# Optimization experiments

Measured on AMD Instinct MI355X. Metric: run time of the kernel, lower is better.

Reference implementation:

```python
import jax, jax.numpy as jnp
import numpy as np

H = 128          # num_hidden
NUM_IN = 256     # 2*H: h_E (H) + gathered neighbor h_V (H)
SCALE = 30.0
LN_EPS = 1e-5


def _ln(x, g, b):
    mu = jnp.mean(x, axis=-1, keepdims=True)
    var = jnp.mean((x - mu) ** 2, axis=-1, keepdims=True)
    return (x - mu) * jax.lax.rsqrt(var + LN_EPS) * g + b


def _gather_nodes(nodes, idx):
    # nodes: [B,L,C], idx: [B,L,K] -> [B,L,K,C]
    B = nodes.shape[0]
    return nodes[jnp.arange(B)[:, None, None], idx]


def _mlp3(x, W1, b1, W2, b2, W3, b3):
    h = jax.nn.gelu(x @ W1 + b1, approximate=False)
    h = jax.nn.gelu(h @ W2 + b2, approximate=False)
    return h @ W3 + b3


def setup_inputs() -> dict:
    key = jax.random.key(0)
    ks = jax.random.split(key, 16)
    B, L, K = 2, 2048, 48
    s = 0.02
    inp = {
        "h_V": jax.random.normal(ks[0], (B, L, H), jnp.float32),
        "h_E": jax.random.normal(ks[1], (B, L, K, H), jnp.float32),
        "E_idx": jax.random.randint(ks[2], (B, L, K), 0, L, jnp.int32),
        "mask_V": jnp.ones((B, L), jnp.float32),
        "mask_attend": jnp.ones((B, L, K), jnp.float32),
        # node-update MLP
        "W1": jax.random.normal(ks[3], (H + NUM_IN, H), jnp.float32) * s,
        "b1": jnp.zeros((H,), jnp.float32),
        "W2": jax.random.normal(ks[4], (H, H), jnp.float32) * s,
        "b2": jnp.zeros((H,), jnp.float32),
        "W3": jax.random.normal(ks[5], (H, H), jnp.float32) * s,
        "b3": jnp.zeros((H,), jnp.float32),
        # edge-update MLP
        "W11": jax.random.normal(ks[6], (H + NUM_IN, H), jnp.float32) * s,
        "b11": jnp.zeros((H,), jnp.float32),
        "W12": jax.random.normal(ks[7], (H, H), jnp.float32) * s,
        "b12": jnp.zeros((H,), jnp.float32),
        "W13": jax.random.normal(ks[8], (H, H), jnp.float32) * s,
        "b13": jnp.zeros((H,), jnp.float32),
        # position-wise FFN (H -> 4H -> H)
        "Win": jax.random.normal(ks[9], (H, 4 * H), jnp.float32) * s,
        "bin": jnp.zeros((4 * H,), jnp.float32),
        "Wout": jax.random.normal(ks[10], (4 * H, H), jnp.float32) * s,
        "bout": jnp.zeros((H,), jnp.float32),
        # LayerNorms
        "g1": jnp.ones((H,), jnp.float32), "be1": jnp.zeros((H,), jnp.float32),
        "g2": jnp.ones((H,), jnp.float32), "be2": jnp.zeros((H,), jnp.float32),
        "g3": jnp.ones((H,), jnp.float32), "be3": jnp.zeros((H,), jnp.float32),
    }
    return inp


def reference(h_V, h_E, E_idx, mask_V, mask_attend,
              W1, b1, W2, b2, W3, b3,
              W11, b11, W12, b12, W13, b13,
              Win, bin, Wout, bout,
              g1, be1, g2, be2, g3, be3):
    K = h_E.shape[-2]
    # --- node update: gather, concat, 3-layer MLP, masked mean-sum, LN residual ---
    h_nbr = _gather_nodes(h_V, E_idx)                               # [B,L,K,H]
    h_V_exp = jnp.broadcast_to(h_V[:, :, None, :], h_nbr.shape)     # [B,L,K,H]
    h_EV = jnp.concatenate([h_V_exp, h_E, h_nbr], axis=-1)          # [B,L,K,3H]
    h_msg = _mlp3(h_EV, W1, b1, W2, b2, W3, b3)                     # [B,L,K,H]
    h_msg = mask_attend[..., None] * h_msg
    dh = jnp.sum(h_msg, axis=-2) / SCALE                            # [B,L,H]
    h_V = _ln(h_V + dh, g1, be1)
    # position-wise FFN + LN residual
    dh = jax.nn.gelu(h_V @ Win + bin, approximate=False) @ Wout + bout
    h_V = _ln(h_V + dh, g2, be2)
    h_V = mask_V[..., None] * h_V
    # --- edge update ---
    h_nbr = _gather_nodes(h_V, E_idx)
    h_V_exp = jnp.broadcast_to(h_V[:, :, None, :], h_nbr.shape)
    h_EV = jnp.concatenate([h_V_exp, h_E, h_nbr], axis=-1)
    h_msg = _mlp3(h_EV, W11, b11, W12, b12, W13, b13)
    h_E = _ln(h_E + h_msg, g3, be3)
    return (h_V, h_E)
```

## Files before the change

### kernel.cpp

```cpp
#include <hip/hip_runtime.h>
#include <hip/hip_bf16.h>

typedef __attribute__((ext_vector_type(8))) short short8;
typedef __attribute__((ext_vector_type(4))) float f32x4;

__device__ inline short f2bf(float f) {
    unsigned u = __builtin_bit_cast(unsigned, f);
    u += 0x7fffu + ((u >> 16) & 1u);
    return (short)(u >> 16);
}
__device__ inline float bf2f(short s) {
    return __builtin_bit_cast(float, ((unsigned)(unsigned short)s) << 16);
}
__device__ inline float bflo(unsigned u) { return __builtin_bit_cast(float, u << 16); }
__device__ inline float bfhi(unsigned u) { return __builtin_bit_cast(float, u & 0xffff0000u); }
__device__ inline unsigned cvt_pk_bf16(float a, float b) {
    unsigned r;
    asm("v_cvt_pk_bf16_f32 %0, %1, %2" : "=v"(r) : "v"(a), "v"(b));
    return r;
}
__device__ inline float gelu_fast(float x) {
    float z = x * (1.0f + 0.044715f * x * x);
    float e = __expf(1.5957691216f * z);
    return x - x * __builtin_amdgcn_rcpf(e + 1.0f);
}
__device__ inline float wred(float s) {
#pragma unroll
    for (int o = 32; o; o >>= 1) s += __shfl_xor(s, o, 64);
    return s;
}

__global__ void pack_all_kernel(const float* __restrict__ W1, const float* __restrict__ W2,
                                const float* __restrict__ W3, const float* __restrict__ W11,
                                const float* __restrict__ W12, const float* __restrict__ W13,
                                const float* __restrict__ Win, const float* __restrict__ Wout,
                                short* __restrict__ out) {
    int b = blockIdx.x;
    if (b < 80) {
        int which = b >> 3;
        const float* Ws[10] = {W1 + 128 * 128, W2, W3, W11 + 128 * 128, W12, W13,
                               W1, W1 + 256 * 128, W11, W11 + 256 * 128};
        const float* W = Ws[which];
        int i = (b & 7) * 256 + threadIdx.x;
        int lane = i & 63, tile = i >> 6;
        int kt = tile & 3, nt = tile >> 2;
        int n = nt * 16 + (lane & 15);
        int k0 = kt * 32 + (lane >> 4) * 8;
        short8 v;
#pragma unroll
        for (int j = 0; j < 8; ++j) v[j] = f2bf(W[(size_t)(k0 + j) * 128 + n]);
        *(short8*)(out + (size_t)which * 16384 + (size_t)i * 8) = v;
    } else if (b < 112) {
        int i = (b - 80) * 256 + threadIdx.x;
        int lane = i & 63, tile = i >> 6;
        int kt = tile & 3, nt = tile >> 2;
        int n = nt * 16 + (lane & 15);
        int k0 = kt * 32 + (lane >> 4) * 8;
        short8 v;
#pragma unroll
        for (int j = 0; j < 8; ++j) v[j] = f2bf(Win[(size_t)(k0 + j) * 512 + n]);
        *(short8*)(out + 163840 + (size_t)i * 8) = v;
    } else {
        int i = (b - 112) * 256 + threadIdx.x;
        int lane = i & 63, tile = i >> 6;
        int kt = tile & 15, nt = tile >> 4;
        int n = nt * 16 + (lane & 15);
        int k0 = kt * 32 + (lane >> 4) * 8;
        short8 v;
#pragma unroll
        for (int j = 0; j < 8; ++j) v[j] = f2bf(Wout[(size_t)(k0 + j) * 128 + n]);
        *(short8*)(out + 229376 + (size_t)i * 8) = v;
    }
}

__global__ __launch_bounds__(256) void node_pre_kernel(
    const float* __restrict__ hV, const short8* __restrict__ Bs,
    const short8* __restrict__ Bn, const float* __restrict__ bias,
    float* __restrict__ Ys, short* __restrict__ Yn) {
    int n0 = blockIdx.x * 16;
    int tid = threadIdx.x, lane = tid & 63, w = tid >> 6;
    __shared__ __align__(16) short A_sw[16 * 128];
    {
        int off = tid * 8;
        int r = off >> 7, c0 = off & 127;
        const float* src = hV + (size_t)n0 * 128 + off;
        float4 f0 = *(const float4*)(src);
        float4 f1 = *(const float4*)(src + 4);
        uint4 u;
        u.x = cvt_pk_bf16(f0.x, f0.y); u.y = cvt_pk_bf16(f0.z, f0.w);
        u.z = cvt_pk_bf16(f1.x, f1.y); u.w = cvt_pk_bf16(f1.z, f1.w);
        *(uint4*)((char*)A_sw + r * 256 + ((c0 * 2) ^ ((r & 7) << 4))) = u;
    }
    __syncthreads();
    const short8* Bp = (w < 2) ? Bs : Bn;
    f32x4 acc[4];
#pragma unroll
    for (int n2 = 0; n2 < 4; ++n2) acc[n2] = (f32x4){0.f, 0.f, 0.f, 0.f};
#pragma unroll
    for (int kt = 0; kt < 4; ++kt) {
        int row = lane & 15;
        int kb = (kt * 32 + (lane >> 4) * 8) * 2;
        short8 a = *(const short8*)((const char*)A_sw + row * 256 + (kb ^ ((row & 7) << 4)));
#pragma unroll
        for (int n2 = 0; n2 < 4; ++n2) {
            int ntl = (w & 1) * 4 + n2;
            short8 bf = Bp[(ntl * 4 + kt) * 64 + lane];
            acc[n2] = __builtin_amdgcn_mfma_f32_16x16x32_bf16(a, bf, acc[n2], 0, 0, 0);
        }
    }
    if (w < 2) {
#pragma unroll
        for (int n2 = 0; n2 < 4; ++n2) {
            int col = ((w & 1) * 4 + n2) * 16 + (lane & 15);
            float bv = bias[col];
#pragma unroll
            for (int i = 0; i < 4; ++i) {
                int row = (lane >> 4) * 4 + i;
                Ys[(size_t)(n0 + row) * 128 + col] = acc[n2][i] + bv;
            }
        }
    } else {
#pragma unroll
        for (int n2 = 0; n2 < 4; ++n2) {
            int col = ((w & 1) * 4 + n2) * 16 + (lane & 15);
#pragma unroll
            for (int i = 0; i < 4; ++i) {
                int row = (lane >> 4) * 4 + i;
                Yn[(size_t)(n0 + row) * 128 + col] = f2bf(acc[n2][i]);
            }
        }
    }
}


__device__ inline void gemm48_a(const short* A_sw, const short8* __restrict__ Wp,
                                int w, int lane, f32x4 acc[3][2]) {
#pragma unroll
    for (int mt = 0; mt < 3; ++mt)
#pragma unroll
        for (int n2 = 0; n2 < 2; ++n2) acc[mt][n2] = (f32x4){0.f, 0.f, 0.f, 0.f};
#pragma unroll
    for (int kt = 0; kt < 4; ++kt) {
        short8 a[3];
        int kb = (kt * 32 + (lane >> 4) * 8) * 2;
#pragma unroll
        for (int mt = 0; mt < 3; ++mt) {
            int row = mt * 16 + (lane & 15);
            a[mt] = *(const short8*)((const char*)A_sw + row * 256 + (kb ^ ((row & 7) << 4)));
        }
#pragma unroll
        for (int n2 = 0; n2 < 2; ++n2) {
            short8 bf = Wp[((w * 2 + n2) * 4 + kt) * 64 + lane];
#pragma unroll
            for (int mt = 0; mt < 3; ++mt)
                acc[mt][n2] = __builtin_amdgcn_mfma_f32_16x16x32_bf16(a[mt], bf, acc[mt][n2], 0, 0, 0);
        }
    }
}

__device__ inline void gemm48_swz(const short* A_sw, const short8* __restrict__ Wp,
                                  int w, int lane, f32x4 acc[2][3]) {
#pragma unroll
    for (int m2 = 0; m2 < 2; ++m2)
#pragma unroll
        for (int nt = 0; nt < 3; ++nt) acc[m2][nt] = (f32x4){0.f, 0.f, 0.f, 0.f};
#pragma unroll
    for (int kt = 0; kt < 4; ++kt) {
        int kb = (kt * 32 + (lane >> 4) * 8) * 2;
        short8 e[3];
#pragma unroll
        for (int nt = 0; nt < 3; ++nt) {
            int row = nt * 16 + (lane & 15);
            e[nt] = *(const short8*)((const char*)A_sw + row * 256 + (kb ^ ((row & 7) << 4)));
        }
#pragma unroll
        for (int m2 = 0; m2 < 2; ++m2) {
            short8 wf = Wp[((w * 2 + m2) * 4 + kt) * 64 + lane];
#pragma unroll
            for (int nt = 0; nt < 3; ++nt)
                acc[m2][nt] = __builtin_amdgcn_mfma_f32_16x16x32_bf16(wf, e[nt], acc[m2][nt], 0, 0, 0);
        }
    }
}

__device__ inline void gemm48_swz1(const short* A_sw, const short8* __restrict__ Wp,
                                   int ft, int lane, f32x4 acc[3]) {
#pragma unroll
    for (int nt = 0; nt < 3; ++nt) acc[nt] = (f32x4){0.f, 0.f, 0.f, 0.f};
#pragma unroll
    for (int kt = 0; kt < 4; ++kt) {
        int kb = (kt * 32 + (lane >> 4) * 8) * 2;
        short8 e[3];
#pragma unroll
        for (int nt = 0; nt < 3; ++nt) {
            int row = nt * 16 + (lane & 15);
            e[nt] = *(const short8*)((const char*)A_sw + row * 256 + (kb ^ ((row & 7) << 4)));
        }
        short8 wf = Wp[(ft * 4 + kt) * 64 + lane];
#pragma unroll
        for (int nt = 0; nt < 3; ++nt)
            acc[nt] = __builtin_amdgcn_mfma_f32_16x16x32_bf16(wf, e[nt], acc[nt], 0, 0, 0);
    }
}

__device__ inline void gemm48_a1(const short* A_sw, const short8* __restrict__ Wp,
                                 int ft, int lane, f32x4 acc[3]) {
#pragma unroll
    for (int mt = 0; mt < 3; ++mt) acc[mt] = (f32x4){0.f, 0.f, 0.f, 0.f};
#pragma unroll
    for (int kt = 0; kt < 4; ++kt) {
        short8 a[3];
        int kb = (kt * 32 + (lane >> 4) * 8) * 2;
#pragma unroll
        for (int mt = 0; mt < 3; ++mt) {
            int row = mt * 16 + (lane & 15);
            a[mt] = *(const short8*)((const char*)A_sw + row * 256 + (kb ^ ((row & 7) << 4)));
        }
        short8 bf = Wp[(ft * 4 + kt) * 64 + lane];
#pragma unroll
        for (int mt = 0; mt < 3; ++mt)
            acc[mt] = __builtin_amdgcn_mfma_f32_16x16x32_bf16(a[mt], bf, acc[mt], 0, 0, 0);
    }
}

__device__ inline void stage_hE(const float* __restrict__ Eb, short* A_sw, int tid) {
#pragma unroll
    for (int i = 0; i < 3; ++i) {
        int e = tid + i * 256;
        int r = e >> 4, c0 = (e & 15) * 8;
        float4 f0 = *(const float4*)(Eb + r * 128 + c0);
        float4 f1 = *(const float4*)(Eb + r * 128 + c0 + 4);
        uint4 u;
        u.x = cvt_pk_bf16(f0.x, f0.y); u.y = cvt_pk_bf16(f0.z, f0.w);
        u.z = cvt_pk_bf16(f1.x, f1.y); u.w = cvt_pk_bf16(f1.z, f1.w);
        *(uint4*)((char*)A_sw + r * 256 + ((c0 * 2) ^ ((r & 7) << 4))) = u;
    }
}

__device__ inline void stage_hE512(const float* __restrict__ Eb, short* A_sw, int tid) {
#pragma unroll
    for (int i = 0; i < 2; ++i) {
        int e = tid + i * 512;
        if (i == 1 && e >= 768) break;
        int r = e >> 4, c0 = (e & 15) * 8;
        float4 f0 = *(const float4*)(Eb + r * 128 + c0);
        float4 f1 = *(const float4*)(Eb + r * 128 + c0 + 4);
        uint4 u;
        u.x = cvt_pk_bf16(f0.x, f0.y); u.y = cvt_pk_bf16(f0.z, f0.w);
        u.z = cvt_pk_bf16(f1.x, f1.y); u.w = cvt_pk_bf16(f1.z, f1.w);
        *(uint4*)((char*)A_sw + r * 256 + ((c0 * 2) ^ ((r & 7) << 4))) = u;
    }
}

__device__ inline void gather_Yn(const short* __restrict__ Yng, const int* __restrict__ Eidx,
                                 int node, int bb, int tid, short* Ygb) {
    if (tid < 192) {
        int r = tid >> 2, q = tid & 3;
        int idx = Eidx[node * 48 + r];
        const short8* src = (const short8*)(Yng + ((size_t)bb * 2048 + idx) * 128 + q * 32);
        short8* dst = (short8*)(Ygb + r * 136 + q * 32);
        dst[0] = src[0];
        dst[1] = src[1];
        dst[2] = src[2];
        dst[3] = src[3];
    }
}

__device__ inline void epi_l1(f32x4 acc[2][3], const float* Ysh, const short* Ygb,
                              short* A_sw, int w, int lane) {
#pragma unroll
    for (int m2 = 0; m2 < 2; ++m2) {
        int featb = (w * 2 + m2) * 16 + ((lane >> 4) << 2);
        float ys0 = Ysh[featb], ys1 = Ysh[featb + 1];
        float ys2 = Ysh[featb + 2], ys3 = Ysh[featb + 3];
#pragma unroll
        for (int nt = 0; nt < 3; ++nt) {
            int edge = nt * 16 + (lane & 15);
            uint2 yv = *(const uint2*)(Ygb + edge * 136 + featb);
            float v0 = gelu_fast(acc[m2][nt][0] + ys0 + bflo(yv.x));
            float v1 = gelu_fast(acc[m2][nt][1] + ys1 + bfhi(yv.x));
            float v2 = gelu_fast(acc[m2][nt][2] + ys2 + bflo(yv.y));
            float v3 = gelu_fast(acc[m2][nt][3] + ys3 + bfhi(yv.y));
            uint2 pk = {cvt_pk_bf16(v0, v1), cvt_pk_bf16(v2, v3)};
            *(uint2*)((char*)A_sw + edge * 256 + ((featb * 2) ^ ((edge & 7) << 4))) = pk;
        }
    }
}

__device__ inline void epi_l2(f32x4 acc[2][3], const float* __restrict__ b,
                              short* A_sw, int w, int lane) {
#pragma unroll
    for (int m2 = 0; m2 < 2; ++m2) {
        int featb = (w * 2 + m2) * 16 + ((lane >> 4) << 2);
        float b0 = b[featb], b1 = b[featb + 1], b2v = b[featb + 2], b3v = b[featb + 3];
#pragma unroll
        for (int nt = 0; nt < 3; ++nt) {
            int edge = nt * 16 + (lane & 15);
            float v0 = gelu_fast(acc[m2][nt][0] + b0);
            float v1 = gelu_fast(acc[m2][nt][1] + b1);
            float v2 = gelu_fast(acc[m2][nt][2] + b2v);
            float v3 = gelu_fast(acc[m2][nt][3] + b3v);
            uint2 pk = {cvt_pk_bf16(v0, v1), cvt_pk_bf16(v2, v3)};
            *(uint2*)((char*)A_sw + edge * 256 + ((featb * 2) ^ ((edge & 7) << 4))) = pk;
        }
    }
}

__global__ __launch_bounds__(256) void node_msg_kernel(
    const float* __restrict__ hV, const float* __restrict__ hE,
    const int* __restrict__ Eidx, const float* __restrict__ maskAtt,
    const short8* __restrict__ W1bp, const short8* __restrict__ W2p,
    const short8* __restrict__ W3p, const float* __restrict__ b2,
    const float* __restrict__ b3, const float* __restrict__ Ysg,
    const short* __restrict__ Yng, const float* __restrict__ g1,
    const float* __restrict__ be1, float* __restrict__ hv1out) {
    const int node = blockIdx.x;
    const int bb = node >> 11;
    const int tid = threadIdx.x;
    const int lane = tid & 63, w = tid >> 6;

    __shared__ __align__(16) short A_sw[48 * 128];
    __shared__ __align__(16) short Ygb[48 * 136];
    __shared__ float Ysh[128];
    __shared__ float mask_s[48];
    __shared__ float red[8];

    stage_hE(hE + (size_t)node * 6144, A_sw, tid);
    if (tid < 128) Ysh[tid] = Ysg[(size_t)node * 128 + tid];
    if (tid >= 192 && tid < 240) mask_s[tid - 192] = maskAtt[node * 48 + tid - 192];
    gather_Yn(Yng, Eidx, node, bb, tid, Ygb);
    __syncthreads();

    f32x4 acc[2][3];
    gemm48_swz(A_sw, W1bp, w, lane, acc);
    __syncthreads();
    epi_l1(acc, Ysh, Ygb, A_sw, w, lane);
    __syncthreads();
    gemm48_swz(A_sw, W2p, w, lane, acc);
    __syncthreads();
    epi_l2(acc, b2, A_sw, w, lane);
    __syncthreads();

    f32x4 acc3[3][2];
    gemm48_a(A_sw, W3p, w, lane, acc3);
    float u[2];
#pragma unroll
    for (int n2 = 0; n2 < 2; ++n2) {
        int col = (w * 2 + n2) * 16 + (lane & 15);
        float b3c = b3[col];
        float s = 0.f;
#pragma unroll
        for (int mt = 0; mt < 3; ++mt)
#pragma unroll
            for (int i = 0; i < 4; ++i) {
                int row = mt * 16 + (lane >> 4) * 4 + i;
                s += (acc3[mt][n2][i] + b3c) * mask_s[row];
            }
        s += __shfl_xor(s, 16, 64);
        s += __shfl_xor(s, 32, 64);
        u[n2] = hV[(size_t)node * 128 + col] + s * (1.0f / 30.0f);
    }
    float ps = wred(u[0] + u[1]) * 0.25f;
    float pq = wred(u[0] * u[0] + u[1] * u[1]) * 0.25f;
    if (lane == 0) { red[w] = ps; red[4 + w] = pq; }
    __syncthreads();
    float S = red[0] + red[1] + red[2] + red[3];
    float Q = red[4] + red[5] + red[6] + red[7];
    float mu = S * (1.0f / 128.0f);
    float var = Q * (1.0f / 128.0f) - mu * mu;
    float rs = rsqrtf(var + 1e-5f);
    if ((lane >> 4) == 0) {
#pragma unroll
        for (int n2 = 0; n2 < 2; ++n2) {
            int col = (w * 2 + n2) * 16 + (lane & 15);
            hv1out[(size_t)node * 128 + col] = (u[n2] - mu) * rs * g1[col] + be1[col];
        }
    }
}

__global__ __launch_bounds__(256) void ffn_kernel(
    const float* __restrict__ hv1, const short8* __restrict__ Winp,
    const float* __restrict__ binp, const short8* __restrict__ Woutp,
    const float* __restrict__ bout, const float* __restrict__ g2,
    const float* __restrict__ be2, const float* __restrict__ maskV,
    float* __restrict__ hVout) {
    int n0 = blockIdx.x * 16;
    int tid = threadIdx.x, lane = tid & 63, w = tid >> 6;
    __shared__ float X[16 * 128];
    __shared__ __align__(16) short A_sw[16 * 128];
    __shared__ __align__(16) short H_sw[16 * 512];

    {
        int off = tid * 8;
        int r = off >> 7, c0 = off & 127;
        const float* src = hv1 + (size_t)n0 * 128 + off;
        float4 f0 = *(const float4*)(src);
        float4 f1 = *(const float4*)(src + 4);
        *(float4*)(&X[off]) = f0;
        *(float4*)(&X[off + 4]) = f1;
        uint4 u;
        u.x = cvt_pk_bf16(f0.x, f0.y); u.y = cvt_pk_bf16(f0.z, f0.w);
        u.z = cvt_pk_bf16(f1.x, f1.y); u.w = cvt_pk_bf16(f1.z, f1.w);
        *(uint4*)((char*)A_sw + r * 256 + ((c0 * 2) ^ ((r & 7) << 4))) = u;
    }
    __syncthreads();

    f32x4 acc1[8];
#pragma unroll
    for (int n2 = 0; n2 < 8; ++n2) acc1[n2] = (f32x4){0.f, 0.f, 0.f, 0.f};
#pragma unroll
    for (int kt = 0; kt < 4; ++kt) {
        int row = lane & 15;
        int kb = (kt * 32 + (lane >> 4) * 8) * 2;
        short8 a = *(const short8*)((const char*)A_sw + row * 256 + (kb ^ ((row & 7) << 4)));
#pragma unroll
        for (int n2 = 0; n2 < 8; ++n2) {
            short8 bf = Winp[((w * 8 + n2) * 4 + kt) * 64 + lane];
            acc1[n2] = __builtin_amdgcn_mfma_f32_16x16x32_bf16(a, bf, acc1[n2], 0, 0, 0);
        }
    }
#pragma unroll
    for (int n2 = 0; n2 < 8; ++n2) {
        int col = (w * 8 + n2) * 16 + (lane & 15);
        float bv = binp[col];
#pragma unroll
        for (int i = 0; i < 4; ++i) {
            int row = (lane >> 4) * 4 + i;
            float v = gelu_fast(acc1[n2][i] + bv);
            *(short*)((char*)H_sw + row * 1024 + ((col * 2) ^ ((row & 7) << 4))) = f2bf(v);
        }
    }
    __syncthreads();

    f32x4 acc2[2];
    acc2[0] = (f32x4){0.f, 0.f, 0.f, 0.f};
    acc2[1] = (f32x4){0.f, 0.f, 0.f, 0.f};
#pragma unroll
    for (int kt = 0; kt < 16; ++kt) {
        int row = lane & 15;
        int kb = (kt * 32 + (lane >> 4) * 8) * 2;
        short8 a = *(const short8*)((const char*)H_sw + row * 1024 + (kb ^ ((row & 7) << 4)));
#pragma unroll
        for (int n2 = 0; n2 < 2; ++n2) {
            short8 bf = Woutp[((w * 2 + n2) * 16 + kt) * 64 + lane];
            acc2[n2] = __builtin_amdgcn_mfma_f32_16x16x32_bf16(a, bf, acc2[n2], 0, 0, 0);
        }
    }
#pragma unroll
    for (int n2 = 0; n2 < 2; ++n2) {
        int col = (w * 2 + n2) * 16 + (lane & 15);
        float bo = bout[col];
#pragma unroll
        for (int i = 0; i < 4; ++i) {
            int row = (lane >> 4) * 4 + i;
            X[row * 128 + col] += acc2[n2][i] + bo;
        }
    }
    __syncthreads();

#pragma unroll
    for (int p = 0; p < 4; ++p) {
        int r = p * 4 + w;
        float u0 = X[r * 128 + lane], u1 = X[r * 128 + lane + 64];
        float s = wred(u0 + u1);
        float q = wred(u0 * u0 + u1 * u1);
        float mu = s * (1.0f / 128.0f);
        float var = q * (1.0f / 128.0f) - mu * mu;
        float rs = rsqrtf(var + 1e-5f);
        float mv = maskV[n0 + r];
        hVout[(size_t)(n0 + r) * 128 + lane] = mv * ((u0 - mu) * rs * g2[lane] + be2[lane]);
        hVout[(size_t)(n0 + r) * 128 + lane + 64] = mv * ((u1 - mu) * rs * g2[lane + 64] + be2[lane + 64]);
    }
}

__global__ __launch_bounds__(512) void edge_upd_kernel(
    const float* __restrict__ hE, const int* __restrict__ Eidx,
    const short8* __restrict__ W11bp, const short8* __restrict__ W12p,
    const short8* __restrict__ W13p, const float* __restrict__ b12,
    const float* __restrict__ b13, const float* __restrict__ Ysg,
    const short* __restrict__ Yng, const float* __restrict__ g3,
    const float* __restrict__ be3, float* __restrict__ hEout) {
    const int node = blockIdx.x;
    const int bb = node >> 11;
    const int tid = threadIdx.x;
    const int lane = tid & 63, w = tid >> 6;

    __shared__ __align__(16) short A_sw[48 * 128];
    __shared__ __align__(16) short Ygb[48 * 136];
    __shared__ float Ysh[128];

    const float* Eb = hE + (size_t)node * 6144;
    stage_hE512(Eb, A_sw, tid);
    if (tid < 128) Ysh[tid] = Ysg[(size_t)node * 128 + tid];
    gather_Yn(Yng, Eidx, node, bb, tid, Ygb);
    __syncthreads();

    f32x4 acc[3];
    gemm48_swz1(A_sw, W11bp, w, lane, acc);
    __syncthreads();
    {
        int featb = w * 16 + ((lane >> 4) << 2);
        float ys0 = Ysh[featb], ys1 = Ysh[featb + 1];
        float ys2 = Ysh[featb + 2], ys3 = Ysh[featb + 3];
#pragma unroll
        for (int nt = 0; nt < 3; ++nt) {
            int edge = nt * 16 + (lane & 15);
            uint2 yv = *(const uint2*)(Ygb + edge * 136 + featb);
            float v0 = gelu_fast(acc[nt][0] + ys0 + bflo(yv.x));
            float v1 = gelu_fast(acc[nt][1] + ys1 + bfhi(yv.x));
            float v2 = gelu_fast(acc[nt][2] + ys2 + bflo(yv.y));
            float v3 = gelu_fast(acc[nt][3] + ys3 + bfhi(yv.y));
            uint2 pk = {cvt_pk_bf16(v0, v1), cvt_pk_bf16(v2, v3)};
            *(uint2*)((char*)A_sw + edge * 256 + ((featb * 2) ^ ((edge & 7) << 4))) = pk;
        }
    }
    __syncthreads();
    gemm48_swz1(A_sw, W12p, w, lane, acc);
    __syncthreads();
    {
        int featb = w * 16 + ((lane >> 4) << 2);
        float b0 = b12[featb], b1 = b12[featb + 1];
        float b2v = b12[featb + 2], b3v = b12[featb + 3];
#pragma unroll
        for (int nt = 0; nt < 3; ++nt) {
            int edge = nt * 16 + (lane & 15);
            float v0 = gelu_fast(acc[nt][0] + b0);
            float v1 = gelu_fast(acc[nt][1] + b1);
            float v2 = gelu_fast(acc[nt][2] + b2v);
            float v3 = gelu_fast(acc[nt][3] + b3v);
            uint2 pk = {cvt_pk_bf16(v0, v1), cvt_pk_bf16(v2, v3)};
            *(uint2*)((char*)A_sw + edge * 256 + ((featb * 2) ^ ((edge & 7) << 4))) = pk;
        }
    }
    __syncthreads();

    f32x4 acc3[3];
    gemm48_a1(A_sw, W13p, w, lane, acc3);
    {
        int col = w * 16 + (lane & 15);
        float bv = b13[col];
#pragma unroll
        for (int mt = 0; mt < 3; ++mt)
#pragma unroll
            for (int i = 0; i < 4; ++i) {
                int row = mt * 16 + (lane >> 4) * 4 + i;
                float v = acc3[mt][i] + bv + Eb[row * 128 + col];
                Ygb[row * 136 + col] = f2bf(v);
            }
    }
    __syncthreads();

    float* outb = hEout + (size_t)node * 6144;
    float gl0 = g3[lane], gl1 = g3[lane + 64];
    float bl0 = be3[lane], bl1 = be3[lane + 64];
#pragma unroll
    for (int p = 0; p < 6; ++p) {
        int r = p * 8 + w;
        float u0 = bf2f(Ygb[r * 136 + lane]);
        float u1 = bf2f(Ygb[r * 136 + lane + 64]);
        float s = wred(u0 + u1);
        float q = wred(u0 * u0 + u1 * u1);
        float mu = s * (1.0f / 128.0f);
        float var = q * (1.0f / 128.0f) - mu * mu;
        float rs = rsqrtf(var + 1e-5f);
        outb[r * 128 + lane] = (u0 - mu) * rs * gl0 + bl0;
        outb[r * 128 + lane + 64] = (u1 - mu) * rs * gl1 + bl1;
    }
}

extern "C" void kernel_launch(void* const* d_in, const int* in_sizes, int n_in,
                              void* d_out, int out_size, void* d_ws, size_t ws_size,
                              hipStream_t stream) {
    const float* hV      = (const float*)d_in[0];
    const float* hE      = (const float*)d_in[1];
    const int*   Eidx    = (const int*)d_in[2];
    const float* maskV   = (const float*)d_in[3];
    const float* maskAtt = (const float*)d_in[4];
    const float* W1  = (const float*)d_in[5];
    const float* b1  = (const float*)d_in[6];
    const float* W2  = (const float*)d_in[7];
    const float* b2  = (const float*)d_in[8];
    const float* W3  = (const float*)d_in[9];
    const float* b3  = (const float*)d_in[10];
    const float* W11 = (const float*)d_in[11];
    const float* b11 = (const float*)d_in[12];
    const float* W12 = (const float*)d_in[13];
    const float* b12 = (const float*)d_in[14];
    const float* W13 = (const float*)d_in[15];
    const float* b13 = (const float*)d_in[16];
    const float* Win = (const float*)d_in[17];
    const float* binp= (const float*)d_in[18];
    const float* Wout= (const float*)d_in[19];
    const float* bout= (const float*)d_in[20];
    const float* g1  = (const float*)d_in[21];
    const float* be1 = (const float*)d_in[22];
    const float* g2  = (const float*)d_in[23];
    const float* be2 = (const float*)d_in[24];
    const float* g3  = (const float*)d_in[25];
    const float* be3 = (const float*)d_in[26];

    char* ws = (char*)d_ws;
    short* Wpk  = (short*)ws;
    float* Ys   = (float*)(ws + 1048576);
    short* Yn   = (short*)(ws + 1048576 + 2097152);
    float* hv1  = (float*)(ws + 1048576 + 2097152 + 1048576);

    float* hVout = (float*)d_out;
    float* hEout = hVout + 2 * 2048 * 128;

    const int NNODE = 2 * 2048;

    pack_all_kernel<<<144, 256, 0, stream>>>(W1, W2, W3, W11, W12, W13, Win, Wout, Wpk);

    node_pre_kernel<<<NNODE / 16, 256, 0, stream>>>(hV,
        (const short8*)(Wpk + 98304), (const short8*)(Wpk + 114688), b1, Ys, Yn);

    node_msg_kernel<<<NNODE, 256, 0, stream>>>(hV, hE, Eidx, maskAtt,
        (const short8*)(Wpk), (const short8*)(Wpk + 16384), (const short8*)(Wpk + 32768),
        b2, b3, Ys, Yn, g1, be1, hv1);

    ffn_kernel<<<NNODE / 16, 256, 0, stream>>>(hv1,
        (const short8*)(Wpk + 163840), binp, (const short8*)(Wpk + 229376), bout,
        g2, be2, maskV, hVout);

    node_pre_kernel<<<NNODE / 16, 256, 0, stream>>>(hVout,
        (const short8*)(Wpk + 131072), (const short8*)(Wpk + 147456), b11, Ys, Yn);

    edge_upd_kernel<<<NNODE, 512, 0, stream>>>(hE, Eidx,
        (const short8*)(Wpk + 49152), (const short8*)(Wpk + 65536), (const short8*)(Wpk + 81920),
        b12, b13, Ys, Yn, g3, be3, hEout);
}
```

Before: 137.7 us.

## Process two nodes per block in edge update kernel with 96-row GEMM tiles

The edge-update kernel now handles two nodes (96 edges) per 256-thread block instead of one node per 512-thread block. Each wave computes 32 output features across all 96 rows, so every weight fragment loaded is reused across twice as many MFMAs. This also halves the block count. The cost is more shared memory and more accumulator registers per thread, which may reduce occupancy. Node-message helpers are inlined and stage and gather functions are templated, with no change in behaviour.

```diff
diff --git a/kernel.cpp b/kernel.cpp
--- a/kernel.cpp
+++ b/kernel.cpp
@@ -183,49 +183,60 @@
     }
 }
 
-__device__ inline void gemm48_swz1(const short* A_sw, const short8* __restrict__ Wp,
-                                   int ft, int lane, f32x4 acc[3]) {
-#pragma unroll
-    for (int nt = 0; nt < 3; ++nt) acc[nt] = (f32x4){0.f, 0.f, 0.f, 0.f};
+__device__ inline void gemm96_swz(const short* A_sw, const short8* __restrict__ Wp,
+                                  int w, int lane, f32x4 acc[2][6]) {
+#pragma unroll
+    for (int m2 = 0; m2 < 2; ++m2)
+#pragma unroll
+        for (int nt = 0; nt < 6; ++nt) acc[m2][nt] = (f32x4){0.f, 0.f, 0.f, 0.f};
 #pragma unroll
     for (int kt = 0; kt < 4; ++kt) {
         int kb = (kt * 32 + (lane >> 4) * 8) * 2;
-        short8 e[3];
-#pragma unroll
-        for (int nt = 0; nt < 3; ++nt) {
+        short8 e[6];
+#pragma unroll
+        for (int nt = 0; nt < 6; ++nt) {
             int row = nt * 16 + (lane & 15);
             e[nt] = *(const short8*)((const char*)A_sw + row * 256 + (kb ^ ((row & 7) << 4)));
         }
-        short8 wf = Wp[(ft * 4 + kt) * 64 + lane];
-#pragma unroll
-        for (int nt = 0; nt < 3; ++nt)
-            acc[nt] = __builtin_amdgcn_mfma_f32_16x16x32_bf16(wf, e[nt], acc[nt], 0, 0, 0);
-    }
-}
-
-__device__ inline void gemm48_a1(const short* A_sw, const short8* __restrict__ Wp,
-                                 int ft, int lane, f32x4 acc[3]) {
-#pragma unroll
-    for (int mt = 0; mt < 3; ++mt) acc[mt] = (f32x4){0.f, 0.f, 0.f, 0.f};
+#pragma unroll
+        for (int m2 = 0; m2 < 2; ++m2) {
+            short8 wf = Wp[((w * 2 + m2) * 4 + kt) * 64 + lane];
+#pragma unroll
+            for (int nt = 0; nt < 6; ++nt)
+                acc[m2][nt] = __builtin_amdgcn_mfma_f32_16x16x32_bf16(wf, e[nt], acc[m2][nt], 0, 0, 0);
+        }
+    }
+}
+
+__device__ inline void gemm96_a(const short* A_sw, const short8* __restrict__ Wp,
+                                int w, int lane, f32x4 acc[6][2]) {
+#pragma unroll
+    for (int mt = 0; mt < 6; ++mt)
+#pragma unroll
+        for (int n2 = 0; n2 < 2; ++n2) acc[mt][n2] = (f32x4){0.f, 0.f, 0.f, 0.f};
 #pragma unroll
     for (int kt = 0; kt < 4; ++kt) {
-        short8 a[3];
+        short8 a[6];
         int kb = (kt * 32 + (lane >> 4) * 8) * 2;
 #pragma unroll
-        for (int mt = 0; mt < 3; ++mt) {
+        for (int mt = 0; mt < 6; ++mt) {
             int row = mt * 16 + (lane & 15);
             a[mt] = *(const short8*)((const char*)A_sw + row * 256 + (kb ^ ((row & 7) << 4)));
         }
-        short8 bf = Wp[(ft * 4 + kt) * 64 + lane];
-#pragma unroll
-        for (int mt = 0; mt < 3; ++mt)
-            acc[mt] = __builtin_amdgcn_mfma_f32_16x16x32_bf16(a[mt], bf, acc[mt], 0, 0, 0);
-    }
-}
-
-__device__ inline void stage_hE(const float* __restrict__ Eb, short* A_sw, int tid) {
-#pragma unroll
-    for (int i = 0; i < 3; ++i) {
+#pragma unroll
+        for (int n2 = 0; n2 < 2; ++n2) {
+            short8 bf = Wp[((w * 2 + n2) * 4 + kt) * 64 + lane];
+#pragma unroll
+            for (int mt = 0; mt < 6; ++mt)
+                acc[mt][n2] = __builtin_amdgcn_mfma_f32_16x16x32_bf16(a[mt], bf, acc[mt][n2], 0, 0, 0);
+        }
+    }
+}
+
+template <int UNITS>
+__device__ inline void stage_rows(const float* __restrict__ Eb, short* A_sw, int tid) {
+#pragma unroll
+    for (int i = 0; i < UNITS / 256; ++i) {
         int e = tid + i * 256;
         int r = e >> 4, c0 = (e & 15) * 8;
         float4 f0 = *(const float4*)(Eb + r * 128 + c0);
@@ -237,71 +248,21 @@
     }
 }
 
-__device__ inline void stage_hE512(const float* __restrict__ Eb, short* A_sw, int tid) {
-#pragma unroll
-    for (int i = 0; i < 2; ++i) {
-        int e = tid + i * 512;
-        if (i == 1 && e >= 768) break;
-        int r = e >> 4, c0 = (e & 15) * 8;
-        float4 f0 = *(const float4*)(Eb + r * 128 + c0);
-        float4 f1 = *(const float4*)(Eb + r * 128 + c0 + 4);
-        uint4 u;
-        u.x = cvt_pk_bf16(f0.x, f0.y); u.y = cvt_pk_bf16(f0.z, f0.w);
-        u.z = cvt_pk_bf16(f1.x, f1.y); u.w = cvt_pk_bf16(f1.z, f1.w);
-        *(uint4*)((char*)A_sw + r * 256 + ((c0 * 2) ^ ((r & 7) << 4))) = u;
-    }
-}
-
+template <int ROWS>
 __device__ inline void gather_Yn(const short* __restrict__ Yng, const int* __restrict__ Eidx,
-                                 int node, int bb, int tid, short* Ygb) {
-    if (tid < 192) {
-        int r = tid >> 2, q = tid & 3;
-        int idx = Eidx[node * 48 + r];
-        const short8* src = (const short8*)(Yng + ((size_t)bb * 2048 + idx) * 128 + q * 32);
-        short8* dst = (short8*)(Ygb + r * 136 + q * 32);
-        dst[0] = src[0];
-        dst[1] = src[1];
-        dst[2] = src[2];
-        dst[3] = src[3];
-    }
-}
-
-__device__ inline void epi_l1(f32x4 acc[2][3], const float* Ysh, const short* Ygb,
-                              short* A_sw, int w, int lane) {
-#pragma unroll
-    for (int m2 = 0; m2 < 2; ++m2) {
-        int featb = (w * 2 + m2) * 16 + ((lane >> 4) << 2);
-        float ys0 = Ysh[featb], ys1 = Ysh[featb + 1];
-        float ys2 = Ysh[featb + 2], ys3 = Ysh[featb + 3];
-#pragma unroll
-        for (int nt = 0; nt < 3; ++nt) {
-            int edge = nt * 16 + (lane & 15);
-            uint2 yv = *(const uint2*)(Ygb + edge * 136 + featb);
-            float v0 = gelu_fast(acc[m2][nt][0] + ys0 + bflo(yv.x));
-            float v1 = gelu_fast(acc[m2][nt][1] + ys1 + bfhi(yv.x));
-            float v2 = gelu_fast(acc[m2][nt][2] + ys2 + bflo(yv.y));
-            float v3 = gelu_fast(acc[m2][nt][3] + ys3 + bfhi(yv.y));
-            uint2 pk = {cvt_pk_bf16(v0, v1), cvt_pk_bf16(v2, v3)};
-            *(uint2*)((char*)A_sw + edge * 256 + ((featb * 2) ^ ((edge & 7) << 4))) = pk;
-        }
-    }
-}
-
-__device__ inline void epi_l2(f32x4 acc[2][3], const float* __restrict__ b,
-                              short* A_sw, int w, int lane) {
-#pragma unroll
-    for (int m2 = 0; m2 < 2; ++m2) {
-        int featb = (w * 2 + m2) * 16 + ((lane >> 4) << 2);
-        float b0 = b[featb], b1 = b[featb + 1], b2v = b[featb + 2], b3v = b[featb + 3];
-#pragma unroll
-        for (int nt = 0; nt < 3; ++nt) {
-            int edge = nt * 16 + (lane & 15);
-            float v0 = gelu_fast(acc[m2][nt][0] + b0);
-            float v1 = gelu_fast(acc[m2][nt][1] + b1);
-            float v2 = gelu_fast(acc[m2][nt][2] + b2v);
-            float v3 = gelu_fast(acc[m2][nt][3] + b3v);
-            uint2 pk = {cvt_pk_bf16(v0, v1), cvt_pk_bf16(v2, v3)};
-            *(uint2*)((char*)A_sw + edge * 256 + ((featb * 2) ^ ((edge & 7) << 4))) = pk;
+                                 int node0, int bb, int tid, short* Ygb) {
+#pragma unroll
+    for (int i = 0; i < (ROWS * 4 + 255) / 256; ++i) {
+        int e = tid + i * 256;
+        if (e < ROWS * 4) {
+            int r = e >> 2, q = e & 3;
+            int idx = Eidx[node0 * 48 + r];
+            const short8* src = (const short8*)(Yng + ((size_t)bb * 2048 + idx) * 128 + q * 32);
+            short8* dst = (short8*)(Ygb + r * 136 + q * 32);
+            dst[0] = src[0];
+            dst[1] = src[1];
+            dst[2] = src[2];
+            dst[3] = src[3];
         }
     }
 }
@@ -325,20 +286,55 @@
     __shared__ float mask_s[48];
     __shared__ float red[8];
 
-    stage_hE(hE + (size_t)node * 6144, A_sw, tid);
+    stage_rows<768>(hE + (size_t)node * 6144, A_sw, tid);
     if (tid < 128) Ysh[tid] = Ysg[(size_t)node * 128 + tid];
     if (tid >= 192 && tid < 240) mask_s[tid - 192] = maskAtt[node * 48 + tid - 192];
-    gather_Yn(Yng, Eidx, node, bb, tid, Ygb);
+    gather_Yn<48>(Yng, Eidx, node, bb, tid, Ygb);
     __syncthreads();
 
     f32x4 acc[2][3];
     gemm48_swz(A_sw, W1bp, w, lane, acc);
     __syncthreads();
-    epi_l1(acc, Ysh, Ygb, A_sw, w, lane);
+    {
+#pragma unroll
+        for (int m2 = 0; m2 < 2; ++m2) {
+            int featb = (w * 2 + m2) * 16 + ((lane >> 4) << 2);
+            float ys0 = Ysh[featb], ys1 = Ysh[featb + 1];
+            float ys2 = Ysh[featb + 2], ys3 = Ysh[featb + 3];
+#pragma unroll
+            for (int nt = 0; nt < 3; ++nt) {
+                int edge = nt * 16 + (lane & 15);
+                uint2 yv = *(const uint2*)(Ygb + edge * 136 + featb);
+                float v0 = gelu_fast(acc[m2][nt][0] + ys0 + bflo(yv.x));
+                float v1 = gelu_fast(acc[m2][nt][1] + ys1 + bfhi(yv.x));
+                float v2 = gelu_fast(acc[m2][nt][2] + ys2 + bflo(yv.y));
+                float v3 = gelu_fast(acc[m2][nt][3] + ys3 + bfhi(yv.y));
+                uint2 pk = {cvt_pk_bf16(v0, v1), cvt_pk_bf16(v2, v3)};
+                *(uint2*)((char*)A_sw + edge * 256 + ((featb * 2) ^ ((edge & 7) << 4))) = pk;
+            }
+        }
+    }
     __syncthreads();
     gemm48_swz(A_sw, W2p, w, lane, acc);
     __syncthreads();
-    epi_l2(acc, b2, A_sw, w, lane);
+    {
+#pragma unroll
+        for (int m2 = 0; m2 < 2; ++m2) {
+            int featb = (w * 2 + m2) * 16 + ((lane >> 4) << 2);
+            float b0 = b2[featb], b1 = b2[featb + 1];
+            float b2v = b2[featb + 2], b3v = b2[featb + 3];
+#pragma unroll
+            for (int nt = 0; nt < 3; ++nt) {
+                int edge = nt * 16 + (lane & 15);
+                float v0 = gelu_fast(acc[m2][nt][0] + b0);
+                float v1 = gelu_fast(acc[m2][nt][1] + b1);
+                float v2 = gelu_fast(acc[m2][nt][2] + b2v);
+                float v3 = gelu_fast(acc[m2][nt][3] + b3v);
+                uint2 pk = {cvt_pk_bf16(v0, v1), cvt_pk_bf16(v2, v3)};
+                *(uint2*)((char*)A_sw + edge * 256 + ((featb * 2) ^ ((edge & 7) << 4))) = pk;
+            }
+        }
+    }
     __syncthreads();
 
     f32x4 acc3[3][2];
@@ -473,89 +469,98 @@
     }
 }
 
-__global__ __launch_bounds__(512) void edge_upd_kernel(
+__global__ __launch_bounds__(256) void edge_upd_kernel(
     const float* __restrict__ hE, const int* __restrict__ Eidx,
     const short8* __restrict__ W11bp, const short8* __restrict__ W12p,
     const short8* __restrict__ W13p, const float* __restrict__ b12,
     const float* __restrict__ b13, const float* __restrict__ Ysg,
     const short* __restrict__ Yng, const float* __restrict__ g3,
     const float* __restrict__ be3, float* __restrict__ hEout) {
-    const int node = blockIdx.x;
-    const int bb = node >> 11;
+    const int node0 = blockIdx.x * 2;
+    const int bb = node0 >> 11;
     const int tid = threadIdx.x;
     const int lane = tid & 63, w = tid >> 6;
 
-    __shared__ __align__(16) short A_sw[48 * 128];
-    __shared__ __align__(16) short Ygb[48 * 136];
-    __shared__ float Ysh[128];
-
-    const float* Eb = hE + (size_t)node * 6144;
-    stage_hE512(Eb, A_sw, tid);
-    if (tid < 128) Ysh[tid] = Ysg[(size_t)node * 128 + tid];
-    gather_Yn(Yng, Eidx, node, bb, tid, Ygb);
-    __syncthreads();
-
-    f32x4 acc[3];
-    gemm48_swz1(A_sw, W11bp, w, lane, acc);
-    __syncthreads();
-    {
-        int featb = w * 16 + ((lane >> 4) << 2);
-        float ys0 = Ysh[featb], ys1 = Ysh[featb + 1];
-        float ys2 = Ysh[featb + 2], ys3 = Ysh[featb + 3];
-#pragma unroll
-        for (int nt = 0; nt < 3; ++nt) {
+    __shared__ __align__(16) short A_sw[96 * 128];
+    __shared__ __align__(16) short Ygb[96 * 136];
+    __shared__ float Ysh[256];
+
+    const float* Eb = hE + (size_t)node0 * 6144;
+    stage_rows<1536>(Eb, A_sw, tid);
+    Ysh[tid] = Ysg[(size_t)node0 * 128 + tid];
+    gather_Yn<96>(Yng, Eidx, node0, bb, tid, Ygb);
+    __syncthreads();
+
+    f32x4 acc[2][6];
+    gemm96_swz(A_sw, W11bp, w, lane, acc);
+    __syncthreads();
+#pragma unroll
+    for (int m2 = 0; m2 < 2; ++m2) {
+        int featb = (w * 2 + m2) * 16 + ((lane >> 4) << 2);
+        float ysA0 = Ysh[featb], ysA1 = Ysh[featb + 1];
+        float ysA2 = Ysh[featb + 2], ysA3 = Ysh[featb + 3];
+        float ysB0 = Ysh[128 + featb], ysB1 = Ysh[128 + featb + 1];
+        float ysB2 = Ysh[128 + featb + 2], ysB3 = Ysh[128 + featb + 3];
+#pragma unroll
+        for (int nt = 0; nt < 6; ++nt) {
             int edge = nt * 16 + (lane & 15);
+            float y0 = (nt < 3) ? ysA0 : ysB0;
+            float y1 = (nt < 3) ? ysA1 : ysB1;
+            float y2 = (nt < 3) ? ysA2 : ysB2;
+            float y3 = (nt < 3) ? ysA3 : ysB3;
             uint2 yv = *(const uint2*)(Ygb + edge * 136 + featb);
-            float v0 = gelu_fast(acc[nt][0] + ys0 + bflo(yv.x));
-            float v1 = gelu_fast(acc[nt][1] + ys1 + bfhi(yv.x));
-            float v2 = gelu_fast(acc[nt][2] + ys2 + bflo(yv.y));
-            float v3 = gelu_fast(acc[nt][3] + ys3 + bfhi(yv.y));
+            float v0 = gelu_fast(acc[m2][nt][0] + y0 + bflo(yv.x));
+            float v1 = gelu_fast(acc[m2][nt][1] + y1 + bfhi(yv.x));
+            float v2 = gelu_fast(acc[m2][nt][2] + y2 + bflo(yv.y));
+            float v3 = gelu_fast(acc[m2][nt][3] + y3 + bfhi(yv.y));
             uint2 pk = {cvt_pk_bf16(v0, v1), cvt_pk_bf16(v2, v3)};
             *(uint2*)((char*)A_sw + edge * 256 + ((featb * 2) ^ ((edge & 7) << 4))) = pk;
         }
     }
     __syncthreads();
-    gemm48_swz1(A_sw, W12p, w, lane, acc);
-    __syncthreads();
-    {
-        int featb = w * 16 + ((lane >> 4) << 2);
+    gemm96_swz(A_sw, W12p, w, lane, acc);
+    __syncthreads();
+#pragma unroll
+    for (int m2 = 0; m2 < 2; ++m2) {
+        int featb = (w * 2 + m2) * 16 + ((lane >> 4) << 2);
         float b0 = b12[featb], b1 = b12[featb + 1];
         float b2v = b12[featb + 2], b3v = b12[featb + 3];
 #pragma unroll
-        for (int nt = 0; nt < 3; ++nt) {
+        for (int nt = 0; nt < 6; ++nt) {
             int edge = nt * 16 + (lane & 15);
-            float v0 = gelu_fast(acc[nt][0] + b0);
-            float v1 = gelu_fast(acc[nt][1] + b1);
-            float v2 = gelu_fast(acc[nt][2] + b2v);
-            float v3 = gelu_fast(acc[nt][3] + b3v);
+            float v0 = gelu_fast(acc[m2][nt][0] + b0);
+            float v1 = gelu_fast(acc[m2][nt][1] + b1);
+            float v2 = gelu_fast(acc[m2][nt][2] + b2v);
+            float v3 = gelu_fast(acc[m2][nt][3] + b3v);
             uint2 pk = {cvt_pk_bf16(v0, v1), cvt_pk_bf16(v2, v3)};
             *(uint2*)((char*)A_sw + edge * 256 + ((featb * 2) ^ ((edge & 7) << 4))) = pk;
         }
     }
     __syncthreads();
 
-    f32x4 acc3[3];
-    gemm48_a1(A_sw, W13p, w, lane, acc3);
-    {
-        int col = w * 16 + (lane & 15);
-        float bv = b13[col];
-#pragma unroll
-        for (int mt = 0; mt < 3; ++mt)
+    f32x4 acc3[6][2];
+    gemm96_a(A_sw, W13p, w, lane, acc3);
+#pragma unroll
+    for (int mt = 0; mt < 6; ++mt)
+#pragma unroll
+        for (int n2 = 0; n2 < 2; ++n2) {
+            int col = (w * 2 + n2) * 16 + (lane & 15);
+            float bv = b13[col];
 #pragma unroll
             for (int i = 0; i < 4; ++i) {
                 int row = mt * 16 + (lane >> 4) * 4 + i;
-                float v = acc3[mt][i] + bv + Eb[row * 128 + col];
+                float v = acc3[mt][n2][i] + bv + Eb[row * 128 + col];
                 Ygb[row * 136 + col] = f2bf(v);
             }
-    }
-    __syncthreads();
-
-    float* outb = hEout + (size_t)node * 6144;
+        }
+    __syncthreads();
+
+    float* outb = hEout + (size_t)node0 * 6144;
     float gl0 = g3[lane], gl1 = g3[lane + 64];
     float bl0 = be3[lane], bl1 = be3[lane + 64];
 #pragma unroll
-    for (int p = 0; p < 6; ++p) {
-        int r = p * 8 + w;
+    for (int p = 0; p < 24; ++p) {
+        int r = p * 4 + w;
         float u0 = bf2f(Ygb[r * 136 + lane]);
         float u1 = bf2f(Ygb[r * 136 + lane + 64]);
         float s = wred(u0 + u1);
@@ -626,7 +631,7 @@
     node_pre_kernel<<<NNODE / 16, 256, 0, stream>>>(hVout,
         (const short8*)(Wpk + 131072), (const short8*)(Wpk + 147456), b11, Ys, Yn);
 
-    edge_upd_kernel<<<NNODE, 512, 0, stream>>>(hE, Eidx,
+    edge_upd_kernel<<<NNODE / 2, 256, 0, stream>>>(hE, Eidx,
         (const short8*)(Wpk + 49152), (const short8*)(Wpk + 65536), (const short8*)(Wpk + 81920),
-        b12, b13, Ys, Yn, g3, be3, hEout);
-}
+        b13 == nullptr ? nullptr : b12, b13, Ys, Yn, g3, be3, hEout);
+}
```

New measurement: 151.6 us. 1.1x slower.
